# Performance work log

Hardware: AMD Instinct MI355X
Metric: run time of the kernel (lower is better)

## Reference

```python
import jax, jax.numpy as jnp
import numpy as np

B, T, C = 8, 1024, 512
H = 8
E = C // 2  # split_idx == per-head dim e


def setup_inputs() -> dict:
    key = jax.random.key(0)
    ks = jax.random.split(key, 6)
    s = 0.02
    return {
        "x": jax.random.normal(ks[0], (B, T, C), dtype=jnp.float32),
        "Wq": jax.random.normal(ks[1], (E * H, E), dtype=jnp.float32) * s,
        "Wk": jax.random.normal(ks[2], (E * H, E), dtype=jnp.float32) * s,
        "Wv": jax.random.normal(ks[3], (E * H, E), dtype=jnp.float32) * s,
        "Wu": jax.random.normal(ks[4], (C - E, E * H), dtype=jnp.float32) * s,
        "bu": jnp.zeros((C - E,), dtype=jnp.float32),
    }


def reference(x, Wq, Wk, Wv, Wu, bu):
    # coupling split: x1 drives attention, x2 gets additive update
    x1 = x[..., :E]           # [B,T,E]
    x2 = x[..., E:]           # [B,T,C-E]
    scale = E ** (-0.25)
    # torch Linear: y = x W^T ; output viewed as (heads, e) -> heads-major rows
    q = jnp.einsum('bti,oi->bto', x1, Wq).reshape(B, T, H, E) * scale
    k = jnp.einsum('bti,oi->bto', x1, Wk).reshape(B, T, H, E) * scale
    v = jnp.einsum('bti,oi->bto', x1, Wv).reshape(B, T, H, E)
    # attention scores [B,H,T,T]
    dot = jnp.einsum('bthe,bshe->bhts', q, k)
    attn = jax.nn.softmax(dot, axis=-1)
    out = jnp.einsum('bhts,bshe->bthe', attn, v).reshape(B, T, H * E)
    unified = jnp.einsum('bto,co->btc', out, Wu) + bu  # [B,T,C-E]
    return jnp.concatenate([x1, x2 + unified], axis=-1)
```

## Files before the change

### kernel.cpp

```cpp
#include <hip/hip_runtime.h>
#include <hip/hip_bf16.h>

#define BB 8
#define TT 1024
#define CC 512
#define HH 8
#define EE 256
#define MM (BB*TT)
#define HE (HH*EE)

using short8 = __attribute__((ext_vector_type(8))) short;
using f32x16 = __attribute__((ext_vector_type(16))) float;
using uint2v = __attribute__((ext_vector_type(2))) unsigned int;

__device__ __forceinline__ unsigned short f2bf(float f) {
  union { float f; unsigned int i; } v; v.f = f;
  unsigned int r = v.i + 0x7FFFu + ((v.i >> 16) & 1u);
  return (unsigned short)(r >> 16);
}
__device__ __forceinline__ unsigned int pk_bf16(float lo, float hi) {
  unsigned int r;
  asm("v_cvt_pk_bf16_f32 %0, %1, %2" : "=v"(r) : "v"(lo), "v"(hi));
  return r;
}
__device__ __forceinline__ void gll16(const void* g, void* l) {
  __builtin_amdgcn_global_load_lds(
      (const __attribute__((address_space(1))) unsigned int*)g,
      (__attribute__((address_space(3))) unsigned int*)l, 16, 0, 0);
}

__global__ __launch_bounds__(256) void prep_kernel(const float* __restrict__ x,
                                                   const float* __restrict__ Wq,
                                                   const float* __restrict__ Wk,
                                                   const float* __restrict__ Wv,
                                                   unsigned short* __restrict__ xb,
                                                   unsigned short* __restrict__ wf,
                                                   float* __restrict__ out) {
  int t = blockIdx.x * 256 + threadIdx.x;
  if (t < 262144) {
    int m = t >> 5;
    int c8 = (t & 31) * 8;
    float4 a = *reinterpret_cast<const float4*>(&x[(size_t)m * CC + c8]);
    float4 b = *reinterpret_cast<const float4*>(&x[(size_t)m * CC + c8 + 4]);
    union { unsigned int u[4]; short8 v; } o;
    o.u[0] = pk_bf16(a.x, a.y); o.u[1] = pk_bf16(a.z, a.w);
    o.u[2] = pk_bf16(b.x, b.y); o.u[3] = pk_bf16(b.z, b.w);
    *reinterpret_cast<short8*>(&xb[(size_t)m * 256 + c8]) = o.v;
    *reinterpret_cast<float4*>(&out[(size_t)m * CC + c8]) = a;
    *reinterpret_cast<float4*>(&out[(size_t)m * CC + c8 + 4]) = b;
  } else {
    int t2 = t - 262144;
    int lane = t2 & 63;
    int rest = t2 >> 6;
    int ks = rest & 15;
    int ng = (rest >> 4) & 63;
    int w = rest >> 10;
    const float* Wp = (w == 0) ? Wq : (w == 1) ? Wk : Wv;
    const float scl = (w == 0) ? 0.25f * 1.44269504089f : (w == 1) ? 0.25f : 1.0f;
    int n = ng * 32 + (lane & 31);
    int e0 = ks * 16 + (lane >> 5) * 8;
    float4 a = *reinterpret_cast<const float4*>(&Wp[(size_t)n * EE + e0]);
    float4 b = *reinterpret_cast<const float4*>(&Wp[(size_t)n * EE + e0 + 4]);
    union { unsigned int u[4]; short8 v; } o;
    o.u[0] = pk_bf16(a.x * scl, a.y * scl); o.u[1] = pk_bf16(a.z * scl, a.w * scl);
    o.u[2] = pk_bf16(b.x * scl, b.y * scl); o.u[3] = pk_bf16(b.z * scl, b.w * scl);
    *reinterpret_cast<short8*>(&wf[(size_t)t2 * 8]) = o.v;
  }
}

__global__ __launch_bounds__(256) void qkv_static_kernel(const unsigned short* __restrict__ xb,
                                                         const unsigned short* __restrict__ wf,
                                                         unsigned short* __restrict__ outq,
                                                         unsigned short* __restrict__ outk,
                                                         unsigned short* __restrict__ outvt) {
  __shared__ unsigned short Ab[64 * 256];

  const int tid = threadIdx.x;
  const int lane = tid & 63;
  const int wid = tid >> 6;
  const int wc = wid;
  const int lo = lane & 31, hi = lane >> 5;

  int bid = blockIdx.x;
  int r = bid >> 3;
  int mt = (bid & 7) * 16 + (r & 15);
  int nt = r >> 4;
  const int m0 = mt * 64;
  const int n0 = nt * 128;

  {
    const int a_sub = lane >> 5;
    const int a_g = lane & 31;
#pragma unroll
    for (int i = 0; i < 8; ++i) {
      int row = 16 * wid + 2 * i + a_sub;
      int gs = a_g ^ (row & 7);
      gll16(xb + (size_t)(m0 + row) * 256 + gs * 8, Ab + (16 * wid + 2 * i) * 256);
    }
  }
  asm volatile("s_waitcnt vmcnt(0)" ::: "memory");
  __builtin_amdgcn_s_barrier();

  f32x16 acc[3][2];
#pragma unroll
  for (int w = 0; w < 3; ++w)
#pragma unroll
    for (int mi = 0; mi < 2; ++mi)
#pragma unroll
      for (int q = 0; q < 16; ++q) acc[w][mi][q] = 0.f;

  const int ng = nt * 4 + wc;
  const short8* wfp = reinterpret_cast<const short8*>(wf);
  const int sxor = lo & 7;

#pragma unroll
  for (int ks = 0; ks < 16; ++ks) {
    short8 bf[3];
#pragma unroll
    for (int w = 0; w < 3; ++w)
      bf[w] = wfp[(size_t)((w * 64 + ng) * 16 + ks) * 64 + lane];
    short8 af[2];
#pragma unroll
    for (int mi = 0; mi < 2; ++mi) {
      int row = 32 * mi + lo;
      int slot = (ks * 2 + hi) ^ sxor;
      af[mi] = *reinterpret_cast<const short8*>(&Ab[row * 256 + slot * 8]);
    }
#pragma unroll
    for (int w = 0; w < 3; ++w)
#pragma unroll
      for (int mi = 0; mi < 2; ++mi)
        acc[w][mi] = __builtin_amdgcn_mfma_f32_32x32x16_bf16(af[mi], bf[w], acc[w][mi], 0, 0, 0);
  }

#pragma unroll
  for (int w = 0; w < 2; ++w) {
    unsigned short* op = (w == 0) ? outq : outk;
#pragma unroll
    for (int mi = 0; mi < 2; ++mi) {
#pragma unroll
      for (int q = 0; q < 16; ++q) {
        int rr = (q & 3) + 8 * (q >> 2) + 4 * hi;
        int m = m0 + 32 * mi + rr;
        int n = n0 + 32 * wc + lo;
        op[(size_t)m * HE + n] = f2bf(acc[w][mi][q]);
      }
    }
  }

  unsigned short* Tr = Ab;
  __syncthreads();
#pragma unroll
  for (int mi = 0; mi < 2; ++mi)
#pragma unroll
    for (int q = 0; q < 16; ++q) {
      int rr = (q & 3) + 8 * (q >> 2) + 4 * hi;
      Tr[(32 * wc + lo) * 72 + 32 * mi + rr] = f2bf(acc[2][mi][q]);
    }
  __syncthreads();
  {
    const int b = m0 >> 10;
    const int t0m = m0 & 1023;
#pragma unroll
    for (int p = 0; p < 4; ++p) {
      int nr = p * 32 + (tid >> 3);
      int chunk = tid & 7;
      int n = n0 + nr;
      size_t drow = ((size_t)b * 8 + (n >> 8)) * 256 + (n & 255);
      *reinterpret_cast<short8*>(&outvt[drow * TT + t0m + chunk * 8]) =
          *reinterpret_cast<const short8*>(&Tr[nr * 72 + chunk * 8]);
    }
  }
}

#define SBLK 32
__global__ __launch_bounds__(256, 2) void attn_kernel(const unsigned short* __restrict__ qg,
                                                      const unsigned short* __restrict__ kg,
                                                      const unsigned short* __restrict__ vtg,
                                                      unsigned short* __restrict__ og) {
  __shared__ char smem[66048];
  unsigned short* Kbuf = (unsigned short*)smem;
  unsigned short* Vbuf = (unsigned short*)(smem + 32768);
  float* lpart = (float*)(smem + 65536);

  const int tid = threadIdx.x;
  const int lane = tid & 63;
  const int wid = tid >> 6;
  const int lo = lane & 31, hi = lane >> 5;

  int logical = (blockIdx.x & 7) * 64 + (blockIdx.x >> 3);
  const int bh = logical >> 3;
  const int t0 = (logical & 7) * 128;
  const int b = bh >> 3, h = bh & 7;
  const size_t qkbase = (size_t)b * TT * HE + (size_t)h * EE;
  const size_t vtbase = (size_t)bh * EE * TT;
  const unsigned short* kg_base = kg + qkbase;
  const unsigned short* vt_base = vtg + vtbase;

  short8 qf[16];
  {
    const unsigned short* qrow = qg + qkbase + (size_t)(t0 + 32 * wid + lo) * HE + hi * 8;
#pragma unroll
    for (int ks = 0; ks < 16; ++ks)
      qf[ks] = *reinterpret_cast<const short8*>(qrow + ks * 16);
  }

  f32x16 Oacc[8];
#pragma unroll
  for (int et = 0; et < 8; ++et)
#pragma unroll
    for (int q = 0; q < 16; ++q) Oacc[et][q] = 0.f;
  float lacc = 0.f;

  const int k_sub = lane >> 5;
  const int k_g   = lane & 31;
  const int v_er  = lane >> 2;
  const int v_g   = lane & 3;
  const int v_gs  = v_g ^ ((lane >> 3) & 3);

#define STAGE_TILE(TIDX, BUF)                                                        \
  {                                                                                  \
    const unsigned short* kt = kg_base + (size_t)(TIDX) * SBLK * HE;                 \
    const unsigned short* vt = vt_base + (size_t)(TIDX) * SBLK;                      \
    unsigned short* Kb = Kbuf + (BUF) * (SBLK * 256);                                \
    unsigned short* Vb = Vbuf + (BUF) * (256 * SBLK);                                \
    _Pragma("unroll")                                                                \
    for (int i = 0; i < 4; ++i) {                                                    \
      int row = 8 * wid + 2 * i + k_sub;                                             \
      int gs = k_g ^ (row & 7);                                                      \
      gll16(kt + (size_t)row * HE + gs * 8, Kb + (8 * wid + 2 * i) * 256);           \
    }                                                                                \
    _Pragma("unroll")                                                                \
    for (int i = 0; i < 4; ++i) {                                                    \
      int row = 64 * wid + 16 * i + v_er;                                            \
      gll16(vt + (size_t)row * TT + v_gs * 8, Vb + (64 * wid + 16 * i) * SBLK);      \
    }                                                                                \
  }

  STAGE_TILE(0, 0)
  asm volatile("s_waitcnt vmcnt(0)" ::: "memory");
  __builtin_amdgcn_s_barrier();
  __builtin_amdgcn_sched_barrier(0);

  for (int t = 0; t < 32; ++t) {
    const int cur = t & 1;
    if (t + 1 < 32) STAGE_TILE(t + 1, cur ^ 1)

    const unsigned short* Kb = Kbuf + cur * (SBLK * 256);
    const unsigned short* Vb = Vbuf + cur * (256 * SBLK);

    f32x16 sacc;
#pragma unroll
    for (int q = 0; q < 16; ++q) sacc[q] = 0.f;
    const int sxor = lo & 7;
#pragma unroll
    for (int ks = 0; ks < 16; ++ks) {
      int slot = (ks * 2 + hi) ^ sxor;
      short8 kf = *reinterpret_cast<const short8*>(&Kb[lo * 256 + slot * 8]);
      sacc = __builtin_amdgcn_mfma_f32_32x32x16_bf16(kf, qf[ks], sacc, 0, 0, 0);
    }

    short8 pa[2];
#pragma unroll
    for (int ksl = 0; ksl < 2; ++ksl) {
      float p0 = __builtin_amdgcn_exp2f(sacc[8 * ksl + 0]);
      float p1 = __builtin_amdgcn_exp2f(sacc[8 * ksl + 1]);
      float p2 = __builtin_amdgcn_exp2f(sacc[8 * ksl + 2]);
      float p3 = __builtin_amdgcn_exp2f(sacc[8 * ksl + 3]);
      float p4 = __builtin_amdgcn_exp2f(sacc[8 * ksl + 4]);
      float p5 = __builtin_amdgcn_exp2f(sacc[8 * ksl + 5]);
      float p6 = __builtin_amdgcn_exp2f(sacc[8 * ksl + 6]);
      float p7 = __builtin_amdgcn_exp2f(sacc[8 * ksl + 7]);
      lacc += ((p0 + p1) + (p2 + p3)) + ((p4 + p5) + (p6 + p7));
      unsigned int a1 = pk_bf16(p0, p1), a2 = pk_bf16(p2, p3);
      unsigned int b1 = pk_bf16(p4, p5), b2 = pk_bf16(p6, p7);
      uint2v r1 = __builtin_amdgcn_permlane32_swap(a1, b1, false, false);
      uint2v r2 = __builtin_amdgcn_permlane32_swap(a2, b2, false, false);
      union { unsigned int u[4]; short8 v; } uu;
      uu.u[0] = r1[0]; uu.u[1] = r2[0]; uu.u[2] = r1[1]; uu.u[3] = r2[1];
      pa[ksl] = uu.v;
    }

    const int vxor = (lo >> 1) & 3;
#pragma unroll
    for (int et = 0; et < 8; ++et) {
      const int erow = et * 32 + lo;
#pragma unroll
      for (int ksl = 0; ksl < 2; ++ksl) {
        int slot = (2 * ksl + hi) ^ vxor;
        short8 vf = *reinterpret_cast<const short8*>(&Vb[erow * SBLK + slot * 8]);
        Oacc[et] = __builtin_amdgcn_mfma_f32_32x32x16_bf16(pa[ksl], vf, Oacc[et], 0, 0, 0);
      }
    }

    asm volatile("s_waitcnt vmcnt(0)" ::: "memory");
    __builtin_amdgcn_s_barrier();
    __builtin_amdgcn_sched_barrier(0);
  }

  lacc += __shfl_xor(lacc, 32);
  if (hi == 0) lpart[wid * 32 + lo] = lacc;
  __syncthreads();
#pragma unroll
  for (int q = 0; q < 16; ++q) {
    int rr = (q & 3) + 8 * (q >> 2) + 4 * hi;
    float inv = 1.0f / lpart[wid * 32 + rr];
    int tq = t0 + 32 * wid + rr;
#pragma unroll
    for (int et = 0; et < 8; ++et)
      og[qkbase + (size_t)tq * HE + et * 32 + lo] = f2bf(Oacc[et][q] * inv);
  }
#undef STAGE_TILE
}

#define PSTR 72
__global__ __launch_bounds__(256) void proj_mfma_kernel(const unsigned short* __restrict__ ao,
                                                        const float* __restrict__ Wu,
                                                        const float* __restrict__ bu,
                                                        const float* __restrict__ x,
                                                        float* __restrict__ out) {
  __shared__ unsigned short As[64 * PSTR];
  __shared__ unsigned short Bs[64 * PSTR];
  const int tid = threadIdx.x;
  const int lane = tid & 63;
  const int wid = tid >> 6;
  const int wr = wid >> 1, wc = wid & 1;
  const int lo = lane & 31, hi = lane >> 5;

  int bid = blockIdx.x;
  int r = bid >> 3;
  int mt = (bid & 7) * 16 + (r & 15);
  int nt = r >> 4;
  const int m0 = mt * 64;
  const int n0 = nt * 64;

  const int arow = tid >> 2;
  const int ag0 = (tid & 3) * 2;
  const int brow = tid >> 2;
  const int bg0 = (tid & 3) * 4;

  short8 raA[2];
  float4 raB[4];
  f32x16 acc;
#pragma unroll
  for (int q = 0; q < 16; ++q) acc[q] = 0.f;

#pragma unroll
  for (int j = 0; j < 2; ++j)
    raA[j] = *reinterpret_cast<const short8*>(&ao[(size_t)(m0 + arow) * HE + (ag0 + j) * 8]);
#pragma unroll
  for (int g = 0; g < 4; ++g)
    raB[g] = *reinterpret_cast<const float4*>(&Wu[(size_t)(n0 + brow) * HE + (bg0 + g) * 4]);

  for (int t = 0; t < 32; ++t) {
#pragma unroll
    for (int j = 0; j < 2; ++j)
      *reinterpret_cast<short8*>(&As[arow * PSTR + (ag0 + j) * 8]) = raA[j];
    {
      union { unsigned int u[4]; short8 v; } w0, w1;
      w0.u[0] = pk_bf16(raB[0].x, raB[0].y); w0.u[1] = pk_bf16(raB[0].z, raB[0].w);
      w0.u[2] = pk_bf16(raB[1].x, raB[1].y); w0.u[3] = pk_bf16(raB[1].z, raB[1].w);
      w1.u[0] = pk_bf16(raB[2].x, raB[2].y); w1.u[1] = pk_bf16(raB[2].z, raB[2].w);
      w1.u[2] = pk_bf16(raB[3].x, raB[3].y); w1.u[3] = pk_bf16(raB[3].z, raB[3].w);
      *reinterpret_cast<short8*>(&Bs[brow * PSTR + ag0 * 8]) = w0.v;
      *reinterpret_cast<short8*>(&Bs[brow * PSTR + (ag0 + 1) * 8]) = w1.v;
    }
    asm volatile("s_waitcnt lgkmcnt(0)" ::: "memory");
    __builtin_amdgcn_s_barrier();
    __builtin_amdgcn_sched_barrier(0);

    if (t + 1 < 32) {
      int k0 = (t + 1) * 64;
#pragma unroll
      for (int j = 0; j < 2; ++j)
        raA[j] = *reinterpret_cast<const short8*>(&ao[(size_t)(m0 + arow) * HE + k0 + (ag0 + j) * 8]);
#pragma unroll
      for (int g = 0; g < 4; ++g)
        raB[g] = *reinterpret_cast<const float4*>(&Wu[(size_t)(n0 + brow) * HE + k0 + (bg0 + g) * 4]);
    }

    __builtin_amdgcn_s_setprio(1);
#pragma unroll
    for (int ks = 0; ks < 4; ++ks) {
      short8 af = *reinterpret_cast<const short8*>(&As[(32 * wr + lo) * PSTR + ks * 16 + hi * 8]);
      short8 bf = *reinterpret_cast<const short8*>(&Bs[(32 * wc + lo) * PSTR + ks * 16 + hi * 8]);
      acc = __builtin_amdgcn_mfma_f32_32x32x16_bf16(af, bf, acc, 0, 0, 0);
    }
    __builtin_amdgcn_s_setprio(0);
    __builtin_amdgcn_s_barrier();
    __builtin_amdgcn_sched_barrier(0);
  }

  {
    int n = n0 + 32 * wc + lo;
    float bias = bu[n];
#pragma unroll
    for (int q = 0; q < 16; ++q) {
      int rr = (q & 3) + 8 * (q >> 2) + 4 * hi;
      int m = m0 + 32 * wr + rr;
      float o = acc[q] + x[(size_t)m * CC + EE + n] + bias;
      out[(size_t)m * CC + EE + n] = o;
    }
  }
}

extern "C" void kernel_launch(void* const* d_in, const int* in_sizes, int n_in,
                              void* d_out, int out_size, void* d_ws, size_t ws_size,
                              hipStream_t stream) {
  const float* x  = (const float*)d_in[0];
  const float* Wq = (const float*)d_in[1];
  const float* Wk = (const float*)d_in[2];
  const float* Wv = (const float*)d_in[3];
  const float* Wu = (const float*)d_in[4];
  const float* bu = (const float*)d_in[5];
  float* out = (float*)d_out;

  unsigned short* q  = (unsigned short*)d_ws;
  unsigned short* k  = q + (size_t)MM * HE;
  unsigned short* vt = k + (size_t)MM * HE;
  unsigned short* ao = vt + (size_t)MM * HE;
  unsigned short* xb = ao;
  unsigned short* wfb = xb + (size_t)MM * EE;

  prep_kernel<<<dim3(1792), dim3(256), 0, stream>>>(x, Wq, Wk, Wv, xb, wfb, out);

  qkv_static_kernel<<<dim3(2048), dim3(256), 0, stream>>>(xb, wfb, q, k, vt);

  attn_kernel<<<dim3(512), dim3(256), 0, stream>>>(q, k, vt, ao);

  proj_mfma_kernel<<<dim3(512), dim3(256), 0, stream>>>(ao, Wu, bu, x, out);
}
```

Before: 154.5 us.

## Software-pipeline attention loop so PV of previous tile overlaps QK^T of current

```diff
diff --git a/kernel.cpp b/kernel.cpp
--- a/kernel.cpp
+++ b/kernel.cpp
@@ -27,6 +27,31 @@
   __builtin_amdgcn_global_load_lds(
       (const __attribute__((address_space(1))) unsigned int*)g,
       (__attribute__((address_space(3))) unsigned int*)l, 16, 0, 0);
+}
+
+__device__ __forceinline__ void softmax_pack(const f32x16& sacc, float& lacc,
+                                             short8& pa0, short8& pa1) {
+  short8 pa[2];
+#pragma unroll
+  for (int ksl = 0; ksl < 2; ++ksl) {
+    float p0 = __builtin_amdgcn_exp2f(sacc[8 * ksl + 0]);
+    float p1 = __builtin_amdgcn_exp2f(sacc[8 * ksl + 1]);
+    float p2 = __builtin_amdgcn_exp2f(sacc[8 * ksl + 2]);
+    float p3 = __builtin_amdgcn_exp2f(sacc[8 * ksl + 3]);
+    float p4 = __builtin_amdgcn_exp2f(sacc[8 * ksl + 4]);
+    float p5 = __builtin_amdgcn_exp2f(sacc[8 * ksl + 5]);
+    float p6 = __builtin_amdgcn_exp2f(sacc[8 * ksl + 6]);
+    float p7 = __builtin_amdgcn_exp2f(sacc[8 * ksl + 7]);
+    lacc += ((p0 + p1) + (p2 + p3)) + ((p4 + p5) + (p6 + p7));
+    unsigned int a1 = pk_bf16(p0, p1), a2 = pk_bf16(p2, p3);
+    unsigned int b1 = pk_bf16(p4, p5), b2 = pk_bf16(p6, p7);
+    uint2v r1 = __builtin_amdgcn_permlane32_swap(a1, b1, false, false);
+    uint2v r2 = __builtin_amdgcn_permlane32_swap(a2, b2, false, false);
+    union { unsigned int u[4]; short8 v; } uu;
+    uu.u[0] = r1[0]; uu.u[1] = r2[0]; uu.u[2] = r1[1]; uu.u[3] = r2[1];
+    pa[ksl] = uu.v;
+  }
+  pa0 = pa[0]; pa1 = pa[1];
 }
 
 __global__ __launch_bounds__(256) void prep_kernel(const float* __restrict__ x,
@@ -215,88 +240,93 @@
   const int k_sub = lane >> 5;
   const int k_g   = lane & 31;
   const int v_er  = lane >> 2;
-  const int v_g   = lane & 3;
-  const int v_gs  = v_g ^ ((lane >> 3) & 3);
-
-#define STAGE_TILE(TIDX, BUF)                                                        \
+  const int v_gs  = (lane & 3) ^ ((lane >> 3) & 3);
+
+#define STAGE_K(TIDX, BUF)                                                           \
   {                                                                                  \
     const unsigned short* kt = kg_base + (size_t)(TIDX) * SBLK * HE;                 \
-    const unsigned short* vt = vt_base + (size_t)(TIDX) * SBLK;                      \
     unsigned short* Kb = Kbuf + (BUF) * (SBLK * 256);                                \
-    unsigned short* Vb = Vbuf + (BUF) * (256 * SBLK);                                \
     _Pragma("unroll")                                                                \
     for (int i = 0; i < 4; ++i) {                                                    \
       int row = 8 * wid + 2 * i + k_sub;                                             \
       int gs = k_g ^ (row & 7);                                                      \
       gll16(kt + (size_t)row * HE + gs * 8, Kb + (8 * wid + 2 * i) * 256);           \
     }                                                                                \
+  }
+#define STAGE_V(TIDX, BUF)                                                           \
+  {                                                                                  \
+    const unsigned short* vt = vt_base + (size_t)(TIDX) * SBLK;                      \
+    unsigned short* Vb = Vbuf + (BUF) * (256 * SBLK);                                \
     _Pragma("unroll")                                                                \
     for (int i = 0; i < 4; ++i) {                                                    \
       int row = 64 * wid + 16 * i + v_er;                                            \
       gll16(vt + (size_t)row * TT + v_gs * 8, Vb + (64 * wid + 16 * i) * SBLK);      \
     }                                                                                \
   }
-
-  STAGE_TILE(0, 0)
+#define QKT(KB, SACC)                                                                \
+  {                                                                                  \
+    const unsigned short* Kb = Kbuf + (KB) * (SBLK * 256);                           \
+    const int sxor = lo & 7;                                                         \
+    _Pragma("unroll")                                                                \
+    for (int ks = 0; ks < 16; ++ks) {                                                \
+      int slot = (ks * 2 + hi) ^ sxor;                                               \
+      short8 kf = *reinterpret_cast<const short8*>(&Kb[lo * 256 + slot * 8]);        \
+      SACC = __builtin_amdgcn_mfma_f32_32x32x16_bf16(kf, qf[ks], SACC, 0, 0, 0);     \
+    }                                                                                \
+  }
+#define PV(VB)                                                                       \
+  {                                                                                  \
+    const unsigned short* Vb = Vbuf + (VB) * (256 * SBLK);                           \
+    const int vxor = (lo >> 1) & 3;                                                  \
+    _Pragma("unroll")                                                                \
+    for (int et = 0; et < 8; ++et) {                                                 \
+      const int erow = et * 32 + lo;                                                 \
+      int slot0 = (0 + hi) ^ vxor;                                                   \
+      int slot1 = (2 + hi) ^ vxor;                                                   \
+      short8 vf0 = *reinterpret_cast<const short8*>(&Vb[erow * SBLK + slot0 * 8]);   \
+      short8 vf1 = *reinterpret_cast<const short8*>(&Vb[erow * SBLK + slot1 * 8]);   \
+      Oacc[et] = __builtin_amdgcn_mfma_f32_32x32x16_bf16(pa0, vf0, Oacc[et], 0, 0, 0); \
+      Oacc[et] = __builtin_amdgcn_mfma_f32_32x32x16_bf16(pa1, vf1, Oacc[et], 0, 0, 0); \
+    }                                                                                \
+  }
+
+  short8 pa0, pa1;
+
+  STAGE_K(0, 0)
   asm volatile("s_waitcnt vmcnt(0)" ::: "memory");
   __builtin_amdgcn_s_barrier();
   __builtin_amdgcn_sched_barrier(0);
 
-  for (int t = 0; t < 32; ++t) {
-    const int cur = t & 1;
-    if (t + 1 < 32) STAGE_TILE(t + 1, cur ^ 1)
-
-    const unsigned short* Kb = Kbuf + cur * (SBLK * 256);
-    const unsigned short* Vb = Vbuf + cur * (256 * SBLK);
-
+  {
+    STAGE_K(1, 1)
+    STAGE_V(0, 0)
     f32x16 sacc;
 #pragma unroll
     for (int q = 0; q < 16; ++q) sacc[q] = 0.f;
-    const int sxor = lo & 7;
-#pragma unroll
-    for (int ks = 0; ks < 16; ++ks) {
-      int slot = (ks * 2 + hi) ^ sxor;
-      short8 kf = *reinterpret_cast<const short8*>(&Kb[lo * 256 + slot * 8]);
-      sacc = __builtin_amdgcn_mfma_f32_32x32x16_bf16(kf, qf[ks], sacc, 0, 0, 0);
-    }
-
-    short8 pa[2];
-#pragma unroll
-    for (int ksl = 0; ksl < 2; ++ksl) {
-      float p0 = __builtin_amdgcn_exp2f(sacc[8 * ksl + 0]);
-      float p1 = __builtin_amdgcn_exp2f(sacc[8 * ksl + 1]);
-      float p2 = __builtin_amdgcn_exp2f(sacc[8 * ksl + 2]);
-      float p3 = __builtin_amdgcn_exp2f(sacc[8 * ksl + 3]);
-      float p4 = __builtin_amdgcn_exp2f(sacc[8 * ksl + 4]);
-      float p5 = __builtin_amdgcn_exp2f(sacc[8 * ksl + 5]);
-      float p6 = __builtin_amdgcn_exp2f(sacc[8 * ksl + 6]);
-      float p7 = __builtin_amdgcn_exp2f(sacc[8 * ksl + 7]);
-      lacc += ((p0 + p1) + (p2 + p3)) + ((p4 + p5) + (p6 + p7));
-      unsigned int a1 = pk_bf16(p0, p1), a2 = pk_bf16(p2, p3);
-      unsigned int b1 = pk_bf16(p4, p5), b2 = pk_bf16(p6, p7);
-      uint2v r1 = __builtin_amdgcn_permlane32_swap(a1, b1, false, false);
-      uint2v r2 = __builtin_amdgcn_permlane32_swap(a2, b2, false, false);
-      union { unsigned int u[4]; short8 v; } uu;
-      uu.u[0] = r1[0]; uu.u[1] = r2[0]; uu.u[2] = r1[1]; uu.u[3] = r2[1];
-      pa[ksl] = uu.v;
-    }
-
-    const int vxor = (lo >> 1) & 3;
-#pragma unroll
-    for (int et = 0; et < 8; ++et) {
-      const int erow = et * 32 + lo;
-#pragma unroll
-      for (int ksl = 0; ksl < 2; ++ksl) {
-        int slot = (2 * ksl + hi) ^ vxor;
-        short8 vf = *reinterpret_cast<const short8*>(&Vb[erow * SBLK + slot * 8]);
-        Oacc[et] = __builtin_amdgcn_mfma_f32_32x32x16_bf16(pa[ksl], vf, Oacc[et], 0, 0, 0);
-      }
-    }
-
+    QKT(0, sacc)
+    softmax_pack(sacc, lacc, pa0, pa1);
     asm volatile("s_waitcnt vmcnt(0)" ::: "memory");
     __builtin_amdgcn_s_barrier();
     __builtin_amdgcn_sched_barrier(0);
   }
+
+  for (int t = 1; t < 32; ++t) {
+    if (t < 31) STAGE_K(t + 1, (t + 1) & 1)
+    STAGE_V(t, t & 1)
+
+    f32x16 sacc;
+#pragma unroll
+    for (int q = 0; q < 16; ++q) sacc[q] = 0.f;
+    QKT(t & 1, sacc)
+    PV((t - 1) & 1)
+    softmax_pack(sacc, lacc, pa0, pa1);
+
+    asm volatile("s_waitcnt vmcnt(0)" ::: "memory");
+    __builtin_amdgcn_s_barrier();
+    __builtin_amdgcn_sched_barrier(0);
+  }
+
+  PV(1)
 
   lacc += __shfl_xor(lacc, 32);
   if (hi == 0) lpart[wid * 32 + lo] = lacc;
@@ -310,7 +340,10 @@
     for (int et = 0; et < 8; ++et)
       og[qkbase + (size_t)tq * HE + et * 32 + lo] = f2bf(Oacc[et][q] * inv);
   }
-#undef STAGE_TILE
+#undef STAGE_K
+#undef STAGE_V
+#undef QKT
+#undef PV
 }
 
 #define PSTR 72
```

Measured after the change: 162.0 us. 1.05x slower.
